# Kernel optimization log

Measured on AMD Instinct MI355X. Metric: run time of the kernel, lower is better.

The kernel has to match this reference:

```python
import jax, jax.numpy as jnp
import numpy as np
import math

N_HEAD = 16
D_MODEL = 1024
ATT_DIM = D_MODEL // N_HEAD


def setup_inputs() -> dict:
    key = jax.random.key(0)
    ks = jax.random.split(key, 11)
    B, T, D = 2, 2048, D_MODEL
    s = 1.0 / math.sqrt(D)
    return {
        "q": jax.random.normal(ks[0], (B, T, D), jnp.float32),
        "k": jax.random.normal(ks[1], (B, T, D), jnp.float32),
        "v": jax.random.normal(ks[2], (B, T, D), jnp.float32),
        "Wq": jax.random.normal(ks[3], (D, D), jnp.float32) * s,
        "bq": jnp.zeros((D,), jnp.float32),
        "Wk": jax.random.normal(ks[4], (D, D), jnp.float32) * s,
        "bk": jnp.zeros((D,), jnp.float32),
        "Wv": jax.random.normal(ks[5], (D, D), jnp.float32) * s,
        "bv": jnp.zeros((D,), jnp.float32),
        "Wo": jax.random.normal(ks[6], (D, D), jnp.float32) * s,
        "bo": jnp.zeros((D,), jnp.float32),
    }


def reference(q, k, v, Wq, bq, Wk, bk, Wv, bv, Wo, bo):
    B, T, D = q.shape
    H, hd = N_HEAD, ATT_DIM
    # Linear projections (torch Linear: x @ W.T + b)
    qh = (q @ Wq.T + bq).reshape(B, T, H, hd).transpose(0, 2, 1, 3)  # [B,H,T,hd]
    kh = (k @ Wk.T + bk).reshape(B, T, H, hd).transpose(0, 2, 1, 3)
    vh = (v @ Wv.T + bv).reshape(B, T, H, hd).transpose(0, 2, 1, 3)
    scale = 1.0 / math.sqrt(hd)
    score = jnp.einsum("bhqd,bhkd->bhqk", qh, kh) * scale  # [B,H,T,T]
    attn = jax.nn.softmax(score, axis=-1)
    out = jnp.einsum("bhqk,bhkd->bhqd", attn, vh)  # [B,H,T,hd]
    out = out.transpose(0, 2, 1, 3).reshape(B, T, D)
    return out @ Wo.T + bo
```

## Files before the change

### kernel.cpp

```cpp
#include <hip/hip_runtime.h>


typedef __attribute__((ext_vector_type(8))) short bf16x8;
typedef __attribute__((ext_vector_type(4))) float f32x4;

#define E22 ((size_t)1 << 22)
#define E20 ((size_t)1 << 20)

__device__ __forceinline__ unsigned short f2bf(float x) {
    unsigned int u = __float_as_uint(x);
    u += 0x7fffu + ((u >> 16) & 1u);
    return (unsigned short)(u >> 16);
}
__device__ __forceinline__ unsigned int pk2bf(float a, float b) {
    return (__float_as_uint(b) & 0xFFFF0000u) | (__float_as_uint(a) >> 16);
}
__device__ __forceinline__ void gl16(const void* g, void* l) {
    __builtin_amdgcn_global_load_lds(
        (const __attribute__((address_space(1))) void*)g,
        (__attribute__((address_space(3))) void*)l, 16, 0, 0);
}
__device__ __forceinline__ f32x4 mfma16(bf16x8 a, bf16x8 b, f32x4 c) {
    return __builtin_amdgcn_mfma_f32_16x16x32_bf16(a, b, c, 0, 0, 0);
}

__global__ __launch_bounds__(256)
void split_all(const float* __restrict__ q, const float* __restrict__ k,
               const float* __restrict__ v, const float* __restrict__ wq,
               const float* __restrict__ wk, const float* __restrict__ wv,
               const float* __restrict__ wo, unsigned short* __restrict__ ws)
{
    const size_t t = (size_t)blockIdx.x * 256 + threadIdx.x;
    const size_t e = t * 4;
    const float* src; unsigned short* dst; size_t off;
    if (e < 3 * E22) {
        const unsigned int which = (unsigned int)(e >> 22);
        src = which == 0 ? q : (which == 1 ? k : v);
        off = e & (E22 - 1);
        dst = ws + (size_t)which * E22;
    } else {
        const size_t e2 = e - 3 * E22;
        const unsigned int which = (unsigned int)(e2 >> 20);
        off = e2 & (E20 - 1);
        src = which == 0 ? wq : (which == 1 ? wk : (which == 2 ? wv : wo));
        dst = ws + 3 * E22 + (size_t)which * E20;
    }
    const float4 xv = *(const float4*)(src + off);
    ushort4 h4;
    h4.x = f2bf(xv.x); h4.y = f2bf(xv.y); h4.z = f2bf(xv.z); h4.w = f2bf(xv.w);
    *(ushort4*)(dst + off) = h4;
}

__global__ __launch_bounds__(256)
void gemm_qkv(const unsigned short* __restrict__ Xall,
              const unsigned short* __restrict__ Wcat,
              const float* __restrict__ bq, const float* __restrict__ bk,
              const float* __restrict__ bv, unsigned short* __restrict__ Qhp,
              unsigned short* __restrict__ Khp, unsigned short* __restrict__ Vtp)
{
    __shared__ unsigned short Xs[4096], Ws[4096];
    const int tid = threadIdx.x;
    const int w = tid >> 6, ln = tid & 63;
    const int quad = ln >> 4, L = ln & 15;
    const int wy = w >> 1, wx = w & 1;

    const int bid = blockIdx.x;
    const int xcd = bid & 7, j = bid >> 3;
    const int gg = xcd * 12 + (j >> 3);
    const int which = gg >> 5, m_i = gg & 31, n_i = j & 7;
    const int m0 = m_i * 128;

    const unsigned short* X = Xall + (size_t)which * E22;
    const unsigned short* W = Wcat + ((size_t)which * 1024 + n_i * 128) * 1024;
    const float* bp = which == 0 ? bq : (which == 1 ? bk : bv);
    unsigned short* outp = which == 0 ? Qhp : (which == 1 ? Khp : Vtp);

    f32x4 acc[4][4];
#pragma unroll
    for (int i = 0; i < 4; ++i)
#pragma unroll
        for (int jj = 0; jj < 4; ++jj) { f32x4 z = {0.f,0.f,0.f,0.f}; acc[i][jj] = z; }

    for (int k0 = 0; k0 < 1024; k0 += 32) {
        __syncthreads();
#pragma unroll
        for (int i = 0; i < 2; ++i) {
            const int ci  = i * 64 + ln;
            const int row = w * 32 + (ci >> 2);
            const int gc  = (ci & 3) ^ ((row >> 1) & 3);
            const size_t goff = (size_t)row * 1024 + k0 + gc * 8;
            const int lb = w * 2048 + i * 1024;
            gl16(X + (size_t)m0 * 1024 + goff, (char*)Xs + lb);
            gl16(W + goff, (char*)Ws + lb);
        }
        __syncthreads();

        bf16x8 ah[4], bh[4];
#pragma unroll
        for (int mt = 0; mt < 4; ++mt) {
            const int row = wy * 64 + mt * 16 + L;
            ah[mt] = *(const bf16x8*)(Xs + row * 32 + ((quad ^ ((row >> 1) & 3)) * 8));
        }
#pragma unroll
        for (int nt = 0; nt < 4; ++nt) {
            const int row = wx * 64 + nt * 16 + L;
            bh[nt] = *(const bf16x8*)(Ws + row * 32 + ((quad ^ ((row >> 1) & 3)) * 8));
        }
#pragma unroll
        for (int mt = 0; mt < 4; ++mt)
#pragma unroll
            for (int nt = 0; nt < 4; ++nt)
                acc[mt][nt] = mfma16(ah[mt], bh[nt], acc[mt][nt]);
    }

#pragma unroll
    for (int mt = 0; mt < 4; ++mt)
#pragma unroll
        for (int nt = 0; nt < 4; ++nt) {
            const int gm0 = m0 + wy * 64 + mt * 16 + quad * 4;
            const int bn  = n_i * 128 + wx * 64 + nt * 16 + L;
            const float bvv = bp[bn];
            const int hh = bn >> 6, dd = bn & 63;
            if (which < 2) {
#pragma unroll
                for (int r = 0; r < 4; ++r) {
                    const int gm = gm0 + r;
                    const int bb = gm >> 11, tt = gm & 2047;
                    outp[((size_t)(bb * 16 + hh) * 2048 + tt) * 64 + dd] =
                        f2bf(acc[mt][nt][r] + bvv);
                }
            } else {
                const int bb = gm0 >> 11, t0 = gm0 & 2047;
                ushort4 pk;
                pk.x = f2bf(acc[mt][nt][0] + bvv);
                pk.y = f2bf(acc[mt][nt][1] + bvv);
                pk.z = f2bf(acc[mt][nt][2] + bvv);
                pk.w = f2bf(acc[mt][nt][3] + bvv);
                *(ushort4*)(outp + ((size_t)(bb * 16 + hh) * 64 + dd) * 2048 + t0) = pk;
            }
        }
}

__global__ __launch_bounds__(256)
void gemm_out(const unsigned short* __restrict__ X, const unsigned short* __restrict__ W,
              const float* __restrict__ bias, float* __restrict__ outp)
{
    __shared__ unsigned short Xs[4096], Ws[2048];
    const int tid = threadIdx.x;
    const int w = tid >> 6, ln = tid & 63;
    const int quad = ln >> 4, L = ln & 15;

    const int bid = blockIdx.x;
    const int xcd = bid & 7, j = bid >> 3;
    const int m0 = (xcd * 4 + (j >> 4)) * 128;
    const int n0 = (j & 15) * 64;

    f32x4 acc[2][4];
#pragma unroll
    for (int i = 0; i < 2; ++i)
#pragma unroll
        for (int jj = 0; jj < 4; ++jj) { f32x4 z = {0.f,0.f,0.f,0.f}; acc[i][jj] = z; }

    for (int k0 = 0; k0 < 1024; k0 += 32) {
        __syncthreads();
#pragma unroll
        for (int i = 0; i < 2; ++i) {
            const int ci  = i * 64 + ln;
            const int row = w * 32 + (ci >> 2);
            const int gc  = (ci & 3) ^ ((row >> 1) & 3);
            const size_t gx = (size_t)(m0 + row) * 1024 + k0 + gc * 8;
            gl16(X + gx, (char*)Xs + w * 2048 + i * 1024);
        }
        {
            const int row = w * 16 + (ln >> 2);
            const int gc  = (ln & 3) ^ ((row >> 1) & 3);
            const size_t gw = (size_t)(n0 + row) * 1024 + k0 + gc * 8;
            gl16(W + gw, (char*)Ws + w * 1024);
        }
        __syncthreads();

        bf16x8 ah[2], bh[4];
#pragma unroll
        for (int mt = 0; mt < 2; ++mt) {
            const int row = w * 32 + mt * 16 + L;
            ah[mt] = *(const bf16x8*)(Xs + row * 32 + ((quad ^ ((row >> 1) & 3)) * 8));
        }
#pragma unroll
        for (int nt = 0; nt < 4; ++nt) {
            const int row = nt * 16 + L;
            bh[nt] = *(const bf16x8*)(Ws + row * 32 + ((quad ^ ((row >> 1) & 3)) * 8));
        }
#pragma unroll
        for (int mt = 0; mt < 2; ++mt)
#pragma unroll
            for (int nt = 0; nt < 4; ++nt)
                acc[mt][nt] = mfma16(ah[mt], bh[nt], acc[mt][nt]);
    }

#pragma unroll
    for (int mt = 0; mt < 2; ++mt)
#pragma unroll
        for (int nt = 0; nt < 4; ++nt) {
            const int gm0 = m0 + w * 32 + mt * 16 + quad * 4;
            const int gn  = n0 + nt * 16 + L;
            const float bvv = bias[gn];
#pragma unroll
            for (int r = 0; r < 4; ++r)
                outp[(size_t)(gm0 + r) * 1024 + gn] = acc[mt][nt][r] + bvv;
        }
}

__global__ __launch_bounds__(256)
void flash(const unsigned short* __restrict__ Qh, const unsigned short* __restrict__ Kh,
           const unsigned short* __restrict__ Vt, unsigned short* __restrict__ A)
{
    __shared__ unsigned short Ks[2][4096], Vs[2][4096];
    __shared__ unsigned short PT[4 * 32 * 72];
    const int tid = threadIdx.x;
    const int w = tid >> 6, ln = tid & 63;
    const int quad = ln >> 4, L = ln & 15;

    const int bid = blockIdx.x;
    const int xcd = bid & 7, j = bid >> 3;
    const int bh_i = xcd * 4 + (j & 3);
    const int qt = j >> 2;
    const int b = bh_i >> 4, h = bh_i & 15;
    const size_t bh = (size_t)bh_i;

    const unsigned short* Qb = Qh + (bh * 2048 + qt * 128 + w * 32) * 64;
    const unsigned short* Kb = Kh + bh * 2048 * 64;
    const unsigned short* Vb = Vt + bh * 64 * 2048;

    bf16x8 bq[2][2];
#pragma unroll
    for (int nt = 0; nt < 2; ++nt)
#pragma unroll
        for (int kc = 0; kc < 2; ++kc)
            bq[nt][kc] = *(const bf16x8*)(Qb + (nt * 16 + L) * 64 + kc * 32 + quad * 8);

    const short one_bf = (short)0x3F80;
    bf16x8 bone = {one_bf, one_bf, one_bf, one_bf, one_bf, one_bf, one_bf, one_bf};

    f32x4 o[4][2];
    f32x4 lacc[2];
#pragma unroll
    for (int mt = 0; mt < 4; ++mt)
#pragma unroll
        for (int nt = 0; nt < 2; ++nt) { f32x4 z = {0.f,0.f,0.f,0.f}; o[mt][nt] = z; }
#pragma unroll
    for (int nt = 0; nt < 2; ++nt) { f32x4 z = {0.f,0.f,0.f,0.f}; lacc[nt] = z; }

    unsigned short* Pw = PT + w * 32 * 72;

    const int ci0 = (w * 2 + 0) * 64 + ln, ci1 = (w * 2 + 1) * 64 + ln;
    const int rr0 = ci0 >> 3, rr1 = ci1 >> 3;
    const int gc0 = (ci0 & 7) ^ (rr0 & 7), gc1 = (ci1 & 7) ^ (rr1 & 7);

#define STAGE(kt_, buf_)                                                        \
    do {                                                                        \
        gl16(Kb + (size_t)((kt_) * 64 + rr0) * 64 + gc0 * 8,                    \
             (char*)Ks[buf_] + (w * 2 + 0) * 1024);                             \
        gl16(Kb + (size_t)((kt_) * 64 + rr1) * 64 + gc1 * 8,                    \
             (char*)Ks[buf_] + (w * 2 + 1) * 1024);                             \
        gl16(Vb + (size_t)rr0 * 2048 + (kt_) * 64 + gc0 * 8,                    \
             (char*)Vs[buf_] + (w * 2 + 0) * 1024);                             \
        gl16(Vb + (size_t)rr1 * 2048 + (kt_) * 64 + gc1 * 8,                    \
             (char*)Vs[buf_] + (w * 2 + 1) * 1024);                             \
    } while (0)

    STAGE(0, 0);

    for (int kt = 0; kt < 32; ++kt) {
        const int cur = kt & 1;
        __syncthreads();
        if (kt < 31) STAGE(kt + 1, cur ^ 1);

        bf16x8 ak[4][2];
#pragma unroll
        for (int mt = 0; mt < 4; ++mt)
#pragma unroll
            for (int kc = 0; kc < 2; ++kc) {
                const int off = (mt * 16 + L) * 64 + (((kc * 4 + quad) ^ (L & 7)) * 8);
                ak[mt][kc] = *(const bf16x8*)(Ks[cur] + off);
            }

        f32x4 s[4][2];
#pragma unroll
        for (int mt = 0; mt < 4; ++mt)
#pragma unroll
            for (int nt = 0; nt < 2; ++nt) {
                f32x4 z = {0.f,0.f,0.f,0.f};
                z = mfma16(ak[mt][0], bq[nt][0], z);
                z = mfma16(ak[mt][1], bq[nt][1], z);
                s[mt][nt] = z;
            }

#pragma unroll
        for (int mt = 0; mt < 4; ++mt)
#pragma unroll
            for (int nt = 0; nt < 2; ++nt) {
                const float p0 = __builtin_amdgcn_exp2f(fmaf(s[mt][nt][0], 0.18033688f, -30.0f));
                const float p1 = __builtin_amdgcn_exp2f(fmaf(s[mt][nt][1], 0.18033688f, -30.0f));
                const float p2 = __builtin_amdgcn_exp2f(fmaf(s[mt][nt][2], 0.18033688f, -30.0f));
                const float p3 = __builtin_amdgcn_exp2f(fmaf(s[mt][nt][3], 0.18033688f, -30.0f));
                uint2 pk2;
                pk2.x = pk2bf(p0, p1);
                pk2.y = pk2bf(p2, p3);
                *(uint2*)(Pw + (nt * 16 + L) * 72 + mt * 16 + quad * 4) = pk2;
            }
        asm volatile("s_waitcnt lgkmcnt(0)" ::: "memory");

        bf16x8 av[4][2], pb[2][2];
#pragma unroll
        for (int mt = 0; mt < 4; ++mt)
#pragma unroll
            for (int kc = 0; kc < 2; ++kc) {
                const int off = (mt * 16 + L) * 64 + (((kc * 4 + quad) ^ (L & 7)) * 8);
                av[mt][kc] = *(const bf16x8*)(Vs[cur] + off);
            }
#pragma unroll
        for (int nt = 0; nt < 2; ++nt)
#pragma unroll
            for (int kc = 0; kc < 2; ++kc)
                pb[nt][kc] = *(const bf16x8*)(Pw + (nt * 16 + L) * 72 + kc * 32 + quad * 8);

#pragma unroll
        for (int mt = 0; mt < 4; ++mt)
#pragma unroll
            for (int nt = 0; nt < 2; ++nt) {
                o[mt][nt] = mfma16(av[mt][0], pb[nt][0], o[mt][nt]);
                o[mt][nt] = mfma16(av[mt][1], pb[nt][1], o[mt][nt]);
            }
#pragma unroll
        for (int nt = 0; nt < 2; ++nt) {
            lacc[nt] = mfma16(bone, pb[nt][0], lacc[nt]);
            lacc[nt] = mfma16(bone, pb[nt][1], lacc[nt]);
        }
    }
#undef STAGE

#pragma unroll
    for (int nt = 0; nt < 2; ++nt) {
        const float inv = 1.0f / lacc[nt][0];
        const int qrow = b * 2048 + qt * 128 + w * 32 + nt * 16 + L;
#pragma unroll
        for (int mt = 0; mt < 4; ++mt) {
            const int d0 = mt * 16 + quad * 4;
            ushort4 pk;
            pk.x = f2bf(o[mt][nt][0] * inv);
            pk.y = f2bf(o[mt][nt][1] * inv);
            pk.z = f2bf(o[mt][nt][2] * inv);
            pk.w = f2bf(o[mt][nt][3] * inv);
            *(ushort4*)(A + (size_t)qrow * 1024 + h * 64 + d0) = pk;
        }
    }
}

extern "C" void kernel_launch(void* const* d_in, const int* in_sizes, int n_in,
                              void* d_out, int out_size, void* d_ws, size_t ws_size,
                              hipStream_t stream) {
    const float* q  = (const float*)d_in[0];
    const float* k  = (const float*)d_in[1];
    const float* v  = (const float*)d_in[2];
    const float* Wq = (const float*)d_in[3];
    const float* bq = (const float*)d_in[4];
    const float* Wk = (const float*)d_in[5];
    const float* bk = (const float*)d_in[6];
    const float* Wv = (const float*)d_in[7];
    const float* bv = (const float*)d_in[8];
    const float* Wo = (const float*)d_in[9];
    const float* bo = (const float*)d_in[10];

    unsigned short* W = (unsigned short*)d_ws;
    unsigned short *Xall = W;
    unsigned short *Wcat = W + 3 * E22;
    unsigned short *Wob  = Wcat + 3 * E20;
    unsigned short *Qhp  = W + 4 * E22;
    unsigned short *Khp  = W + 5 * E22;
    unsigned short *Vtp  = W + 6 * E22;
    unsigned short *A    = W;

    split_all<<<16384, 256, 0, stream>>>(q, k, v, Wq, Wk, Wv, Wo, W);

    gemm_qkv<<<768, 256, 0, stream>>>(Xall, Wcat, bq, bk, bv, Qhp, Khp, Vtp);

    flash<<<512, 256, 0, stream>>>(Qhp, Khp, Vtp, A);

    gemm_out<<<512, 256, 0, stream>>>(A, Wob, bo, (float*)d_out);
}
```

Baseline: 237.2 us.

## Load K/V directly from global into registers in flash, fold softmax scale into Q

The flash kernel drops its LDS double-buffered K/V staging and per-tile __syncthreads. Each wave now reads K (prefetched one tile ahead in registers) and V directly from global memory, so the only LDS left is the per-wave P buffer, whose row pitch is padded to 76. The softmax scale is folded into the Q projection epilogue, and the constant -30 offset is dropped, which removes an FMA per score but risks exp2 overflow for large scores. It also adds launch_bounds(256,2) and swaps the bf16 pack for a v_perm, trading shared-memory reuse of K/V across the four waves for redundant global/L2 traffic.

Result: slower. 299.6 us (+26.3%).

```diff
diff --git a/kernel.cpp b/kernel.cpp
--- a/kernel.cpp
+++ b/kernel.cpp
@@ -13,7 +13,7 @@
     return (unsigned short)(u >> 16);
 }
 __device__ __forceinline__ unsigned int pk2bf(float a, float b) {
-    return (__float_as_uint(b) & 0xFFFF0000u) | (__float_as_uint(a) >> 16);
+    return __builtin_amdgcn_perm(__float_as_uint(a), __float_as_uint(b), 0x03020706u);
 }
 __device__ __forceinline__ void gl16(const void* g, void* l) {
     __builtin_amdgcn_global_load_lds(
@@ -74,6 +74,7 @@
     const unsigned short* W = Wcat + ((size_t)which * 1024 + n_i * 128) * 1024;
     const float* bp = which == 0 ? bq : (which == 1 ? bk : bv);
     unsigned short* outp = which == 0 ? Qhp : (which == 1 ? Khp : Vtp);
+    const float qscale = which == 0 ? 0.18033688011f : 1.0f;
 
     f32x4 acc[4][4];
 #pragma unroll
@@ -127,7 +128,7 @@
                     const int gm = gm0 + r;
                     const int bb = gm >> 11, tt = gm & 2047;
                     outp[((size_t)(bb * 16 + hh) * 2048 + tt) * 64 + dd] =
-                        f2bf(acc[mt][nt][r] + bvv);
+                        f2bf((acc[mt][nt][r] + bvv) * qscale);
                 }
             } else {
                 const int bb = gm0 >> 11, t0 = gm0 & 2047;
@@ -210,12 +211,11 @@
         }
 }
 
-__global__ __launch_bounds__(256)
+__global__ __launch_bounds__(256, 2)
 void flash(const unsigned short* __restrict__ Qh, const unsigned short* __restrict__ Kh,
            const unsigned short* __restrict__ Vt, unsigned short* __restrict__ A)
 {
-    __shared__ unsigned short Ks[2][4096], Vs[2][4096];
-    __shared__ unsigned short PT[4 * 32 * 72];
+    __shared__ unsigned short PT[4 * 32 * 76];
     const int tid = threadIdx.x;
     const int w = tid >> 6, ln = tid & 63;
     const int quad = ln >> 4, L = ln & 15;
@@ -225,11 +225,10 @@
     const int bh_i = xcd * 4 + (j & 3);
     const int qt = j >> 2;
     const int b = bh_i >> 4, h = bh_i & 15;
-    const size_t bh = (size_t)bh_i;
-
-    const unsigned short* Qb = Qh + (bh * 2048 + qt * 128 + w * 32) * 64;
-    const unsigned short* Kb = Kh + bh * 2048 * 64;
-    const unsigned short* Vb = Vt + bh * 64 * 2048;
+
+    const unsigned short* Qb = Qh + ((size_t)bh_i * 2048 + qt * 128 + w * 32) * 64;
+    const unsigned short* Kb = Kh + (size_t)bh_i * 2048 * 64;
+    const unsigned short* Vb = Vt + (size_t)bh_i * 64 * 2048;
 
     bf16x8 bq[2][2];
 #pragma unroll
@@ -238,6 +237,15 @@
         for (int kc = 0; kc < 2; ++kc)
             bq[nt][kc] = *(const bf16x8*)(Qb + (nt * 16 + L) * 64 + kc * 32 + quad * 8);
 
+    int koff[4][2], voff[4][2];
+#pragma unroll
+    for (int mt = 0; mt < 4; ++mt)
+#pragma unroll
+        for (int kc = 0; kc < 2; ++kc) {
+            koff[mt][kc] = (mt * 16 + L) * 64 + kc * 32 + quad * 8;
+            voff[mt][kc] = (mt * 16 + L) * 2048 + kc * 32 + quad * 8;
+        }
+
     const short one_bf = (short)0x3F80;
     bf16x8 bone = {one_bf, one_bf, one_bf, one_bf, one_bf, one_bf, one_bf, one_bf};
 
@@ -250,38 +258,27 @@
 #pragma unroll
     for (int nt = 0; nt < 2; ++nt) { f32x4 z = {0.f,0.f,0.f,0.f}; lacc[nt] = z; }
 
-    unsigned short* Pw = PT + w * 32 * 72;
-
-    const int ci0 = (w * 2 + 0) * 64 + ln, ci1 = (w * 2 + 1) * 64 + ln;
-    const int rr0 = ci0 >> 3, rr1 = ci1 >> 3;
-    const int gc0 = (ci0 & 7) ^ (rr0 & 7), gc1 = (ci1 & 7) ^ (rr1 & 7);
-
-#define STAGE(kt_, buf_)                                                        \
-    do {                                                                        \
-        gl16(Kb + (size_t)((kt_) * 64 + rr0) * 64 + gc0 * 8,                    \
-             (char*)Ks[buf_] + (w * 2 + 0) * 1024);                             \
-        gl16(Kb + (size_t)((kt_) * 64 + rr1) * 64 + gc1 * 8,                    \
-             (char*)Ks[buf_] + (w * 2 + 1) * 1024);                             \
-        gl16(Vb + (size_t)rr0 * 2048 + (kt_) * 64 + gc0 * 8,                    \
-             (char*)Vs[buf_] + (w * 2 + 0) * 1024);                             \
-        gl16(Vb + (size_t)rr1 * 2048 + (kt_) * 64 + gc1 * 8,                    \
-             (char*)Vs[buf_] + (w * 2 + 1) * 1024);                             \
-    } while (0)
-
-    STAGE(0, 0);
-
+    unsigned short* Pw = PT + w * 32 * 76;
+
+    bf16x8 ak[2][4][2], av[4][2];
+#pragma unroll
+    for (int mt = 0; mt < 4; ++mt)
+#pragma unroll
+        for (int kc = 0; kc < 2; ++kc)
+            ak[0][mt][kc] = *(const bf16x8*)(Kb + koff[mt][kc]);
+
+#pragma unroll 2
     for (int kt = 0; kt < 32; ++kt) {
         const int cur = kt & 1;
-        __syncthreads();
-        if (kt < 31) STAGE(kt + 1, cur ^ 1);
-
-        bf16x8 ak[4][2];
+        const unsigned short* Kn = Kb + ((kt + 1) & 31) * 4096;
+        const unsigned short* Vk = Vb + kt * 64;
+
 #pragma unroll
         for (int mt = 0; mt < 4; ++mt)
 #pragma unroll
             for (int kc = 0; kc < 2; ++kc) {
-                const int off = (mt * 16 + L) * 64 + (((kc * 4 + quad) ^ (L & 7)) * 8);
-                ak[mt][kc] = *(const bf16x8*)(Ks[cur] + off);
+                ak[cur ^ 1][mt][kc] = *(const bf16x8*)(Kn + koff[mt][kc]);
+                av[mt][kc]          = *(const bf16x8*)(Vk + voff[mt][kc]);
             }
 
         f32x4 s[4][2];
@@ -290,8 +287,8 @@
 #pragma unroll
             for (int nt = 0; nt < 2; ++nt) {
                 f32x4 z = {0.f,0.f,0.f,0.f};
-                z = mfma16(ak[mt][0], bq[nt][0], z);
-                z = mfma16(ak[mt][1], bq[nt][1], z);
+                z = mfma16(ak[cur][mt][0], bq[nt][0], z);
+                z = mfma16(ak[cur][mt][1], bq[nt][1], z);
                 s[mt][nt] = z;
             }
 
@@ -299,30 +296,23 @@
         for (int mt = 0; mt < 4; ++mt)
 #pragma unroll
             for (int nt = 0; nt < 2; ++nt) {
-                const float p0 = __builtin_amdgcn_exp2f(fmaf(s[mt][nt][0], 0.18033688f, -30.0f));
-                const float p1 = __builtin_amdgcn_exp2f(fmaf(s[mt][nt][1], 0.18033688f, -30.0f));
-                const float p2 = __builtin_amdgcn_exp2f(fmaf(s[mt][nt][2], 0.18033688f, -30.0f));
-                const float p3 = __builtin_amdgcn_exp2f(fmaf(s[mt][nt][3], 0.18033688f, -30.0f));
+                const float p0 = __builtin_amdgcn_exp2f(s[mt][nt][0]);
+                const float p1 = __builtin_amdgcn_exp2f(s[mt][nt][1]);
+                const float p2 = __builtin_amdgcn_exp2f(s[mt][nt][2]);
+                const float p3 = __builtin_amdgcn_exp2f(s[mt][nt][3]);
                 uint2 pk2;
                 pk2.x = pk2bf(p0, p1);
                 pk2.y = pk2bf(p2, p3);
-                *(uint2*)(Pw + (nt * 16 + L) * 72 + mt * 16 + quad * 4) = pk2;
+                *(uint2*)(Pw + (nt * 16 + L) * 76 + mt * 16 + quad * 4) = pk2;
             }
         asm volatile("s_waitcnt lgkmcnt(0)" ::: "memory");
 
-        bf16x8 av[4][2], pb[2][2];
-#pragma unroll
-        for (int mt = 0; mt < 4; ++mt)
-#pragma unroll
-            for (int kc = 0; kc < 2; ++kc) {
-                const int off = (mt * 16 + L) * 64 + (((kc * 4 + quad) ^ (L & 7)) * 8);
-                av[mt][kc] = *(const bf16x8*)(Vs[cur] + off);
-            }
+        bf16x8 pb[2][2];
 #pragma unroll
         for (int nt = 0; nt < 2; ++nt)
 #pragma unroll
             for (int kc = 0; kc < 2; ++kc)
-                pb[nt][kc] = *(const bf16x8*)(Pw + (nt * 16 + L) * 72 + kc * 32 + quad * 8);
+                pb[nt][kc] = *(const bf16x8*)(Pw + (nt * 16 + L) * 76 + kc * 32 + quad * 8);
 
 #pragma unroll
         for (int mt = 0; mt < 4; ++mt)
@@ -337,7 +327,6 @@
             lacc[nt] = mfma16(bone, pb[nt][1], lacc[nt]);
         }
     }
-#undef STAGE
 
 #pragma unroll
     for (int nt = 0; nt < 2; ++nt) {
```
